# Kernel tuning notes

Hardware: AMD Instinct MI355X
Metric: run time of the kernel (lower is better)

The kernel has to match this reference:

```python
import jax, jax.numpy as jnp
import numpy as np

FEATURES = 2048
BATCH = 16384
N_PAIRS = FEATURES * (FEATURES - 1) // 2  # 2,096,128


def setup_inputs() -> dict:
    key = jax.random.key(0)
    k1, k2, k3, k4 = jax.random.split(key, 4)
    x = jax.random.normal(k1, (BATCH, FEATURES), dtype=jnp.float32)
    # original torch.rand initializers -> uniform [0, 1)
    w0 = jax.random.uniform(k2, (1, 1), dtype=jnp.float32)
    w = jax.random.uniform(k3, (FEATURES, 1), dtype=jnp.float32)
    bw = jax.random.uniform(k4, (N_PAIRS, 1), dtype=jnp.float32)
    return {"x": x, "w0": w0, "w": w, "bw": bw}


def reference(x, w0, w, bw):
    # Pairwise cross term: sum_{j1<j2} bw[i] * x[:, j1] * x[:, j2]
    # Loop order (j1 outer, j2 inner, j1 < j2) is exactly the row-major
    # strictly-upper-triangle order of jnp.triu_indices(k=1).
    F = x.shape[1]
    iu = jnp.triu_indices(F, k=1)
    B = jnp.zeros((F, F), dtype=x.dtype).at[iu].set(bw[:, 0])  # [F, F]
    cross = jnp.einsum('bi,ij,bj->b', x, B, x)[:, None]        # [batch, 1]
    logits = x @ w + w0 + cross                                 # [batch, 1]
    return jax.nn.sigmoid(logits)
```

## Files before the change

### kernel.cpp

```cpp
#include <hip/hip_runtime.h>
#include <hip/hip_bf16.h>

#define F 2048
#define MBATCH 16384
#define BM 256
#define BN 256
#define BK 32
#define PL (BM * BK)
#define THREADS 512

typedef short bf16x8 __attribute__((ext_vector_type(8)));
typedef float f32x4 __attribute__((ext_vector_type(4)));

static __device__ __forceinline__ unsigned short bfb(float v) {
    return __builtin_bit_cast(unsigned short, __float2bfloat16(v));
}
static __device__ __forceinline__ float bff(unsigned short u) {
    return __bfloat162float(__builtin_bit_cast(__hip_bfloat16, u));
}
static __device__ __forceinline__ unsigned pack_hi16(float a, float b) {
    return __builtin_amdgcn_perm(__builtin_bit_cast(unsigned, b),
                                 __builtin_bit_cast(unsigned, a), 0x07060302u);
}
static __device__ __forceinline__ float trunc_hi(float v) {
    return __builtin_bit_cast(float, __builtin_bit_cast(unsigned, v) & 0xffff0000u);
}
static __device__ __forceinline__ unsigned cvtpk_bf16(float a, float b) {
    unsigned r;
    asm("v_cvt_pk_bf16_f32 %0, %1, %2" : "=v"(r) : "v"(a), "v"(b));
    return r;
}

__global__ __launch_bounds__(256) void build_bt(const float* __restrict__ bw,
                                                unsigned short* __restrict__ bt_hi,
                                                unsigned short* __restrict__ bt_lo) {
    __shared__ unsigned short tH[64][72], tL[64][72];
    const int bx = blockIdx.x & 31;
    const int by = blockIdx.x >> 5;
    const int r  = threadIdx.x >> 2;
    const int cg = (threadIdx.x & 3) * 16;
    const bool up = (by >= bx);
    if (up) {
        int j1 = bx * 64 + r;
        long base = (long)j1 * F - (((long)j1 * (j1 + 1)) >> 1) - j1 - 1;
#pragma unroll
        for (int c = 0; c < 16; ++c) {
            int j2 = by * 64 + cg + c;
            float v = (j2 > j1) ? bw[base + j2] : 0.f;
            unsigned short h = bfb(v);
            tH[r][cg + c] = h;
            tL[r][cg + c] = bfb(v - bff(h));
        }
    }
    __syncthreads();
    size_t obase = (size_t)(by * 64 + r) * F + bx * 64 + cg;
    uint4 H0 = {0,0,0,0}, H1 = {0,0,0,0}, L0 = {0,0,0,0}, L1 = {0,0,0,0};
    if (up) {
        unsigned oh[16], ol[16];
#pragma unroll
        for (int c = 0; c < 16; ++c) { oh[c] = tH[cg + c][r]; ol[c] = tL[cg + c][r]; }
        H0.x = oh[0] | (oh[1] << 16);  H0.y = oh[2] | (oh[3] << 16);
        H0.z = oh[4] | (oh[5] << 16);  H0.w = oh[6] | (oh[7] << 16);
        H1.x = oh[8] | (oh[9] << 16);  H1.y = oh[10] | (oh[11] << 16);
        H1.z = oh[12] | (oh[13] << 16); H1.w = oh[14] | (oh[15] << 16);
        L0.x = ol[0] | (ol[1] << 16);  L0.y = ol[2] | (ol[3] << 16);
        L0.z = ol[4] | (ol[5] << 16);  L0.w = ol[6] | (ol[7] << 16);
        L1.x = ol[8] | (ol[9] << 16);  L1.y = ol[10] | (ol[11] << 16);
        L1.z = ol[12] | (ol[13] << 16); L1.w = ol[14] | (ol[15] << 16);
    }
    *(uint4*)(bt_hi + obase)     = H0;
    *(uint4*)(bt_hi + obase + 8) = H1;
    *(uint4*)(bt_lo + obase)     = L0;
    *(uint4*)(bt_lo + obase + 8) = L1;
}

__global__ __launch_bounds__(THREADS, 2) void poly2_gemm(
        const float* __restrict__ x,
        const unsigned short* __restrict__ bt_hi,
        const unsigned short* __restrict__ bt_lo,
        const float* __restrict__ w,
        float* __restrict__ cross_acc) {
    extern __shared__ unsigned short smem[];

    const int tid  = threadIdx.x;
    const int lane = tid & 63;
    const int wid  = tid >> 6;
    const int wm   = wid >> 2;
    const int wn   = wid & 3;
    const int lr   = lane & 15;
    const int lg   = lane >> 4;

    const int g  = blockIdx.x >> 6;
    const int nt = (g < 4) ? (7 - g) : (g - 4);
    const int mt = blockIdx.x & 63;
    const int m0 = mt * BM;
    const int n0 = nt * BN;
    const int ktiles = 8 * (nt + 1);

    f32x4 acc[8][4] = {};

    auto stageB = [&](int buf, int k0) {
        unsigned short* Bh = smem + buf * 4 * PL + 2 * PL;
        unsigned short* Bl = Bh + PL;
#pragma unroll
        for (int it = 0; it < 2; ++it) {
            int q  = it * THREADS + tid;
            int rp = q >> 3, s = q & 7;
            int h  = s ^ (rp & 7);
            int col  = n0 + 2 * rp + (h >> 2);
            int koff = k0 + (h & 3) * 8;
            const unsigned short* ghi = bt_hi + (size_t)col * F + koff;
            const unsigned short* glo = bt_lo + (size_t)col * F + koff;
            unsigned short* dh = Bh + (q & ~63) * 8;
            unsigned short* dl = Bl + (q & ~63) * 8;
            __builtin_amdgcn_global_load_lds(
                (const __attribute__((address_space(1))) unsigned int*)ghi,
                (__attribute__((address_space(3))) unsigned int*)dh, 16, 0, 0);
            __builtin_amdgcn_global_load_lds(
                (const __attribute__((address_space(1))) unsigned int*)glo,
                (__attribute__((address_space(3))) unsigned int*)dl, 16, 0, 0);
        }
    };
    auto loadA = [&](int k0, float4* raw) {
#pragma unroll
        for (int hf = 0; hf < 2; ++hf) {
            int q  = hf * THREADS + tid;
            int rp = q >> 3, s = q & 7;
            int h  = s ^ (rp & 7);
            const float* src = x + (size_t)(m0 + 2 * rp + (h >> 2)) * F + k0 + (h & 3) * 8;
            raw[hf * 2 + 0] = ((const float4*)src)[0];
            raw[hf * 2 + 1] = ((const float4*)src)[1];
        }
    };
    auto writeA = [&](int buf, const float4* raw) {
        unsigned short* Ah = smem + buf * 4 * PL;
        unsigned short* Al = Ah + PL;
#pragma unroll
        for (int hf = 0; hf < 2; ++hf) {
            int q = hf * THREADS + tid;
            float e0 = raw[hf*2].x, e1 = raw[hf*2].y, e2 = raw[hf*2].z, e3 = raw[hf*2].w;
            float e4 = raw[hf*2+1].x, e5 = raw[hf*2+1].y, e6 = raw[hf*2+1].z, e7 = raw[hf*2+1].w;
            uint4 H, L;
            H.x = pack_hi16(e0, e1); H.y = pack_hi16(e2, e3);
            H.z = pack_hi16(e4, e5); H.w = pack_hi16(e6, e7);
            L.x = cvtpk_bf16(e0 - trunc_hi(e0), e1 - trunc_hi(e1));
            L.y = cvtpk_bf16(e2 - trunc_hi(e2), e3 - trunc_hi(e3));
            L.z = cvtpk_bf16(e4 - trunc_hi(e4), e5 - trunc_hi(e5));
            L.w = cvtpk_bf16(e6 - trunc_hi(e6), e7 - trunc_hi(e7));
            *(uint4*)&Ah[q * 8] = H;
            *(uint4*)&Al[q * 8] = L;
        }
    };
    auto compute = [&](int buf) {
        const unsigned short* Ah = smem + buf * 4 * PL;
        const unsigned short* Al = Ah + PL;
        const unsigned short* Bh = Al + PL;
        const unsigned short* Bl = Bh + PL;
        bf16x8 bh[4], bl[4];
#pragma unroll
        for (int n = 0; n < 4; ++n) {
            int c  = wn * 64 + n * 16 + lr;
            int rp = c >> 1;
            int off = rp * 64 + ((((c & 1) << 2) + lg) ^ (rp & 7)) * 8;
            bh[n] = *(const bf16x8*)&Bh[off];
            bl[n] = *(const bf16x8*)&Bl[off];
        }
#pragma unroll
        for (int mh = 0; mh < 2; ++mh) {
            bf16x8 ah[4], al[4];
#pragma unroll
            for (int m2 = 0; m2 < 4; ++m2) {
                int r  = wm * 128 + (mh * 4 + m2) * 16 + lr;
                int rp = r >> 1;
                int off = rp * 64 + ((((r & 1) << 2) + lg) ^ (rp & 7)) * 8;
                ah[m2] = *(const bf16x8*)&Ah[off];
                al[m2] = *(const bf16x8*)&Al[off];
            }
#pragma unroll
            for (int m2 = 0; m2 < 4; ++m2)
#pragma unroll
                for (int n = 0; n < 4; ++n) {
                    f32x4 c0 = acc[mh * 4 + m2][n];
                    c0 = __builtin_amdgcn_mfma_f32_16x16x32_bf16(ah[m2], bh[n], c0, 0, 0, 0);
                    c0 = __builtin_amdgcn_mfma_f32_16x16x32_bf16(ah[m2], bl[n], c0, 0, 0, 0);
                    c0 = __builtin_amdgcn_mfma_f32_16x16x32_bf16(al[m2], bh[n], c0, 0, 0, 0);
                    acc[mh * 4 + m2][n] = c0;
                }
        }
    };

    {
        float4 raw[4];
        stageB(0, 0);
        loadA(0, raw);
        writeA(0, raw);
    }
    __syncthreads();

    int cur = 0;
    for (int kt = 0; kt < ktiles; ++kt) {
        const bool more = (kt + 1) < ktiles;
        float4 raw[4];
        if (more) {
            stageB(cur ^ 1, (kt + 1) * BK);
            loadA((kt + 1) * BK, raw);
        }
        compute(cur);
        if (more) writeA(cur ^ 1, raw);
        __syncthreads();
        cur ^= 1;
    }

#pragma unroll
    for (int m = 0; m < 8; ++m) {
#pragma unroll
        for (int r = 0; r < 4; ++r) {
            int grow = m0 + wm * 128 + m * 16 + lg * 4 + r;
            float sum = 0.f;
#pragma unroll
            for (int n = 0; n < 4; ++n) {
                int gcol = n0 + wn * 64 + n * 16 + lr;
                float yv = acc[m][n][r] + w[gcol];
                sum += yv * x[(size_t)grow * F + gcol];
            }
            sum += __shfl_xor(sum, 1);
            sum += __shfl_xor(sum, 2);
            sum += __shfl_xor(sum, 4);
            sum += __shfl_xor(sum, 8);
            if (lr == 0) atomicAdd(&cross_acc[grow], sum);
        }
    }
}

__global__ __launch_bounds__(256) void finish_sigmoid(const float* __restrict__ cross,
                                                      const float* __restrict__ w0,
                                                      float* __restrict__ out) {
    int b = blockIdx.x * 256 + threadIdx.x;
    float z = cross[b] + w0[0];
    out[b] = 1.f / (1.f + expf(-z));
}

extern "C" void kernel_launch(void* const* d_in, const int* in_sizes, int n_in,
                              void* d_out, int out_size, void* d_ws, size_t ws_size,
                              hipStream_t stream) {
    const float* x  = (const float*)d_in[0];
    const float* w0 = (const float*)d_in[1];
    const float* w  = (const float*)d_in[2];
    const float* bw = (const float*)d_in[3];
    float* out = (float*)d_out;

    float* cross = (float*)d_ws;
    unsigned short* bt_hi = (unsigned short*)((char*)d_ws + (size_t)MBATCH * sizeof(float));
    unsigned short* bt_lo = bt_hi + (size_t)F * F;

    hipFuncSetAttribute((const void*)poly2_gemm,
                        hipFuncAttributeMaxDynamicSharedMemorySize, 131072);

    hipMemsetAsync(cross, 0, (size_t)MBATCH * sizeof(float), stream);
    build_bt<<<(F / 64) * (F / 64), 256, 0, stream>>>(bw, bt_hi, bt_lo);
    poly2_gemm<<<(MBATCH / BM) * (F / BN), THREADS, 131072, stream>>>(x, bt_hi, bt_lo, w, cross);
    finish_sigmoid<<<MBATCH / 256, 256, 0, stream>>>(cross, w0, out);
}
```

Before: 392.6 us.

## Split K-tile compute into four barrier-separated phases interleaving loads with MFMA

Restructures the main loop into four quadrant phases, each reading a subset of A/B fragments from LDS and issuing part of the next tile's global loads or LDS writes before running that quadrant's MFMAs. Workgroup barriers with s_setprio raise priority during MFMA bursts, in a ping-pong style schedule. The goal is to overlap memory traffic with matrix math and shrink register pressure from holding all fragments at once. It adds several extra barriers per K-tile, and B fragments are reread once more per tile.

```diff
diff --git a/kernel.cpp b/kernel.cpp
--- a/kernel.cpp
+++ b/kernel.cpp
@@ -99,117 +99,132 @@
 
     f32x4 acc[8][4] = {};
 
-    auto stageB = [&](int buf, int k0) {
+    auto stageB_it = [&](int buf, int k0, int it) {
         unsigned short* Bh = smem + buf * 4 * PL + 2 * PL;
         unsigned short* Bl = Bh + PL;
-#pragma unroll
-        for (int it = 0; it < 2; ++it) {
-            int q  = it * THREADS + tid;
-            int rp = q >> 3, s = q & 7;
-            int h  = s ^ (rp & 7);
-            int col  = n0 + 2 * rp + (h >> 2);
-            int koff = k0 + (h & 3) * 8;
-            const unsigned short* ghi = bt_hi + (size_t)col * F + koff;
-            const unsigned short* glo = bt_lo + (size_t)col * F + koff;
-            unsigned short* dh = Bh + (q & ~63) * 8;
-            unsigned short* dl = Bl + (q & ~63) * 8;
-            __builtin_amdgcn_global_load_lds(
-                (const __attribute__((address_space(1))) unsigned int*)ghi,
-                (__attribute__((address_space(3))) unsigned int*)dh, 16, 0, 0);
-            __builtin_amdgcn_global_load_lds(
-                (const __attribute__((address_space(1))) unsigned int*)glo,
-                (__attribute__((address_space(3))) unsigned int*)dl, 16, 0, 0);
-        }
-    };
-    auto loadA = [&](int k0, float4* raw) {
-#pragma unroll
-        for (int hf = 0; hf < 2; ++hf) {
-            int q  = hf * THREADS + tid;
-            int rp = q >> 3, s = q & 7;
-            int h  = s ^ (rp & 7);
-            const float* src = x + (size_t)(m0 + 2 * rp + (h >> 2)) * F + k0 + (h & 3) * 8;
-            raw[hf * 2 + 0] = ((const float4*)src)[0];
-            raw[hf * 2 + 1] = ((const float4*)src)[1];
-        }
-    };
-    auto writeA = [&](int buf, const float4* raw) {
+        int q  = it * THREADS + tid;
+        int rp = q >> 3, s = q & 7;
+        int h  = s ^ (rp & 7);
+        int col  = n0 + 2 * rp + (h >> 2);
+        int koff = k0 + (h & 3) * 8;
+        const unsigned short* ghi = bt_hi + (size_t)col * F + koff;
+        const unsigned short* glo = bt_lo + (size_t)col * F + koff;
+        unsigned short* dh = Bh + (q & ~63) * 8;
+        unsigned short* dl = Bl + (q & ~63) * 8;
+        __builtin_amdgcn_global_load_lds(
+            (const __attribute__((address_space(1))) unsigned int*)ghi,
+            (__attribute__((address_space(3))) unsigned int*)dh, 16, 0, 0);
+        __builtin_amdgcn_global_load_lds(
+            (const __attribute__((address_space(1))) unsigned int*)glo,
+            (__attribute__((address_space(3))) unsigned int*)dl, 16, 0, 0);
+    };
+    auto loadA_it = [&](int k0, int it, float4& a, float4& b) {
+        int q  = it * THREADS + tid;
+        int rp = q >> 3, s = q & 7;
+        int h  = s ^ (rp & 7);
+        const float* src = x + (size_t)(m0 + 2 * rp + (h >> 2)) * F + k0 + (h & 3) * 8;
+        a = ((const float4*)src)[0];
+        b = ((const float4*)src)[1];
+    };
+    auto writeA_it = [&](int buf, int it, float4 a, float4 b) {
         unsigned short* Ah = smem + buf * 4 * PL;
         unsigned short* Al = Ah + PL;
-#pragma unroll
-        for (int hf = 0; hf < 2; ++hf) {
-            int q = hf * THREADS + tid;
-            float e0 = raw[hf*2].x, e1 = raw[hf*2].y, e2 = raw[hf*2].z, e3 = raw[hf*2].w;
-            float e4 = raw[hf*2+1].x, e5 = raw[hf*2+1].y, e6 = raw[hf*2+1].z, e7 = raw[hf*2+1].w;
-            uint4 H, L;
-            H.x = pack_hi16(e0, e1); H.y = pack_hi16(e2, e3);
-            H.z = pack_hi16(e4, e5); H.w = pack_hi16(e6, e7);
-            L.x = cvtpk_bf16(e0 - trunc_hi(e0), e1 - trunc_hi(e1));
-            L.y = cvtpk_bf16(e2 - trunc_hi(e2), e3 - trunc_hi(e3));
-            L.z = cvtpk_bf16(e4 - trunc_hi(e4), e5 - trunc_hi(e5));
-            L.w = cvtpk_bf16(e6 - trunc_hi(e6), e7 - trunc_hi(e7));
-            *(uint4*)&Ah[q * 8] = H;
-            *(uint4*)&Al[q * 8] = L;
-        }
-    };
-    auto compute = [&](int buf) {
-        const unsigned short* Ah = smem + buf * 4 * PL;
+        int q = it * THREADS + tid;
+        uint4 H, L;
+        H.x = pack_hi16(a.x, a.y); H.y = pack_hi16(a.z, a.w);
+        H.z = pack_hi16(b.x, b.y); H.w = pack_hi16(b.z, b.w);
+        L.x = cvtpk_bf16(a.x - trunc_hi(a.x), a.y - trunc_hi(a.y));
+        L.y = cvtpk_bf16(a.z - trunc_hi(a.z), a.w - trunc_hi(a.w));
+        L.z = cvtpk_bf16(b.x - trunc_hi(b.x), b.y - trunc_hi(b.y));
+        L.w = cvtpk_bf16(b.z - trunc_hi(b.z), b.w - trunc_hi(b.w));
+        *(uint4*)&Ah[q * 8] = H;
+        *(uint4*)&Al[q * 8] = L;
+    };
+    auto readA = [&](const unsigned short* Ah, const unsigned short* Al,
+                     int mh, bf16x8* ah, bf16x8* al) {
+#pragma unroll
+        for (int m2 = 0; m2 < 4; ++m2) {
+            int r  = wm * 128 + mh * 64 + m2 * 16 + lr;
+            int rp = r >> 1;
+            int off = rp * 64 + ((((r & 1) << 2) + lg) ^ (rp & 7)) * 8;
+            ah[m2] = *(const bf16x8*)&Ah[off];
+            al[m2] = *(const bf16x8*)&Al[off];
+        }
+    };
+    auto readB = [&](const unsigned short* Bh, const unsigned short* Bl,
+                     int nh, bf16x8* bh, bf16x8* bl) {
+#pragma unroll
+        for (int j = 0; j < 2; ++j) {
+            int c  = wn * 64 + (nh * 2 + j) * 16 + lr;
+            int rp = c >> 1;
+            int off = rp * 64 + ((((c & 1) << 2) + lg) ^ (rp & 7)) * 8;
+            bh[j] = *(const bf16x8*)&Bh[off];
+            bl[j] = *(const bf16x8*)&Bl[off];
+        }
+    };
+    auto quad = [&](int mh, int nh, const bf16x8* ah, const bf16x8* al,
+                    const bf16x8* bh, const bf16x8* bl) {
+#pragma unroll
+        for (int m2 = 0; m2 < 4; ++m2)
+#pragma unroll
+            for (int j = 0; j < 2; ++j) {
+                int n = nh * 2 + j;
+                f32x4 c0 = acc[mh * 4 + m2][n];
+                c0 = __builtin_amdgcn_mfma_f32_16x16x32_bf16(ah[m2], bh[j], c0, 0, 0, 0);
+                c0 = __builtin_amdgcn_mfma_f32_16x16x32_bf16(ah[m2], bl[j], c0, 0, 0, 0);
+                c0 = __builtin_amdgcn_mfma_f32_16x16x32_bf16(al[m2], bh[j], c0, 0, 0, 0);
+                acc[mh * 4 + m2][n] = c0;
+            }
+    };
+
+#define PHASE_GO()  do { __builtin_amdgcn_s_barrier();                         \
+                         asm volatile("s_waitcnt lgkmcnt(0)" ::: "memory");    \
+                         __builtin_amdgcn_sched_barrier(0);                    \
+                         __builtin_amdgcn_s_setprio(1); } while (0)
+#define PHASE_END() do { __builtin_amdgcn_s_setprio(0);                        \
+                         __builtin_amdgcn_s_barrier(); } while (0)
+
+    {
+        float4 a0, b0, a1, b1;
+        stageB_it(0, 0, 0); stageB_it(0, 0, 1);
+        loadA_it(0, 0, a0, b0); loadA_it(0, 1, a1, b1);
+        writeA_it(0, 0, a0, b0); writeA_it(0, 1, a1, b1);
+    }
+    __syncthreads();
+
+    int cur = 0;
+    for (int kt = 0; kt < ktiles; ++kt) {
+        const bool more = (kt + 1) < ktiles;
+        const int k1 = (kt + 1) * BK;
+        const unsigned short* Ah = smem + cur * 4 * PL;
         const unsigned short* Al = Ah + PL;
         const unsigned short* Bh = Al + PL;
         const unsigned short* Bl = Bh + PL;
-        bf16x8 bh[4], bl[4];
-#pragma unroll
-        for (int n = 0; n < 4; ++n) {
-            int c  = wn * 64 + n * 16 + lr;
-            int rp = c >> 1;
-            int off = rp * 64 + ((((c & 1) << 2) + lg) ^ (rp & 7)) * 8;
-            bh[n] = *(const bf16x8*)&Bh[off];
-            bl[n] = *(const bf16x8*)&Bl[off];
-        }
-#pragma unroll
-        for (int mh = 0; mh < 2; ++mh) {
-            bf16x8 ah[4], al[4];
-#pragma unroll
-            for (int m2 = 0; m2 < 4; ++m2) {
-                int r  = wm * 128 + (mh * 4 + m2) * 16 + lr;
-                int rp = r >> 1;
-                int off = rp * 64 + ((((r & 1) << 2) + lg) ^ (rp & 7)) * 8;
-                ah[m2] = *(const bf16x8*)&Ah[off];
-                al[m2] = *(const bf16x8*)&Al[off];
-            }
-#pragma unroll
-            for (int m2 = 0; m2 < 4; ++m2)
-#pragma unroll
-                for (int n = 0; n < 4; ++n) {
-                    f32x4 c0 = acc[mh * 4 + m2][n];
-                    c0 = __builtin_amdgcn_mfma_f32_16x16x32_bf16(ah[m2], bh[n], c0, 0, 0, 0);
-                    c0 = __builtin_amdgcn_mfma_f32_16x16x32_bf16(ah[m2], bl[n], c0, 0, 0, 0);
-                    c0 = __builtin_amdgcn_mfma_f32_16x16x32_bf16(al[m2], bh[n], c0, 0, 0, 0);
-                    acc[mh * 4 + m2][n] = c0;
-                }
-        }
-    };
-
-    {
-        float4 raw[4];
-        stageB(0, 0);
-        loadA(0, raw);
-        writeA(0, raw);
-    }
-    __syncthreads();
-
-    int cur = 0;
-    for (int kt = 0; kt < ktiles; ++kt) {
-        const bool more = (kt + 1) < ktiles;
-        float4 raw[4];
-        if (more) {
-            stageB(cur ^ 1, (kt + 1) * BK);
-            loadA((kt + 1) * BK, raw);
-        }
-        compute(cur);
-        if (more) writeA(cur ^ 1, raw);
+        bf16x8 ah[4], al[4], bh[2], bl[2];
+        float4 r0a, r0b, r1a, r1b;
+
+        readA(Ah, Al, 0, ah, al);
+        readB(Bh, Bl, 0, bh, bl);
+        if (more) { stageB_it(cur ^ 1, k1, 0); loadA_it(k1, 0, r0a, r0b); }
+        PHASE_GO();  quad(0, 0, ah, al, bh, bl);  PHASE_END();
+
+        readB(Bh, Bl, 1, bh, bl);
+        if (more) { stageB_it(cur ^ 1, k1, 1); loadA_it(k1, 1, r1a, r1b); }
+        PHASE_GO();  quad(0, 1, ah, al, bh, bl);  PHASE_END();
+
+        readA(Ah, Al, 1, ah, al);
+        if (more) writeA_it(cur ^ 1, 0, r0a, r0b);
+        PHASE_GO();  quad(1, 1, ah, al, bh, bl);  PHASE_END();
+
+        readB(Bh, Bl, 0, bh, bl);
+        if (more) writeA_it(cur ^ 1, 1, r1a, r1b);
+        PHASE_GO();  quad(1, 0, ah, al, bh, bl);
+        __builtin_amdgcn_s_setprio(0);
         __syncthreads();
         cur ^= 1;
     }
+#undef PHASE_GO
+#undef PHASE_END
 
 #pragma unroll
     for (int m = 0; m < 8; ++m) {
```

After: 457.9 us. +16.6%, slower.
